# Kernel optimization log

Measured on AMD Instinct MI355X. Metric: run time of the kernel, lower is better.

## Reference

```python
import jax, jax.numpy as jnp
import numpy as np

NEG_SLOPE = 0.1

def _leaky(x):
    return jnp.where(x >= 0, x, NEG_SLOPE * x)

def setup_inputs() -> dict:
    key = jax.random.key(0)
    ks = jax.random.split(key, 16)
    B, N, H, W, C = 4, 128, 32, 32, 64
    inp = {
        "image": jax.random.normal(ks[0], (B, 3, H, W), dtype=jnp.float32),
        "coords": jax.random.uniform(ks[1], (B, N, 2), dtype=jnp.float32),
        "w1": jax.random.normal(ks[2], (C, 7), dtype=jnp.float32) * 0.2,
        "b1": jax.random.normal(ks[3], (C,), dtype=jnp.float32) * 0.05,
        "w2": jax.random.normal(ks[4], (C, C), dtype=jnp.float32) * 0.1,
        "b2": jax.random.normal(ks[5], (C,), dtype=jnp.float32) * 0.05,
        "w3": jax.random.normal(ks[6], (C, C), dtype=jnp.float32) * 0.1,
        "b3": jax.random.normal(ks[7], (C,), dtype=jnp.float32) * 0.05,
        "w4": jax.random.normal(ks[8], (C, C), dtype=jnp.float32) * 0.1,
        "b4": jax.random.normal(ks[9], (C,), dtype=jnp.float32) * 0.05,
        "w5": jax.random.normal(ks[10], (C, C), dtype=jnp.float32) * 0.1,
        "b5": jax.random.normal(ks[11], (C,), dtype=jnp.float32) * 0.05,
        "wl": jax.random.normal(ks[12], (3, C), dtype=jnp.float32) * 0.1,
        "bl": jax.random.normal(ks[13], (3,), dtype=jnp.float32) * 0.05,
    }
    return inp

def reference(image, coords, w1, b1, w2, b2, w3, b3, w4, b4, w5, b5, wl, bl):
    B, C_img, H, W = image.shape
    _, N, D = coords.shape
    # position encoding: channel 0 = row/(H-1), channel 1 = col/(W-1)
    row = (jnp.arange(H, dtype=jnp.float32) / (H - 1))[:, None] * jnp.ones((1, W), jnp.float32)
    col = jnp.ones((H, 1), jnp.float32) * (jnp.arange(W, dtype=jnp.float32) / (W - 1))[None, :]
    pos = jnp.stack([row, col], axis=0)  # [2,H,W]
    # x5: [B,5,H,W] = image ++ pos
    x5 = jnp.concatenate([image, jnp.broadcast_to(pos[None], (B, 2, H, W))], axis=1)
    # First 1x1 conv: split weight into image/pos part (5 ch) and coord part (2 ch);
    # avoids materializing the expanded [B*N,7,H,W] input (same math as conv on concat).
    img_part = jnp.einsum('oc,bchw->bohw', w1[:, :5], x5)          # [B,c,H,W]
    crd_part = jnp.einsum('od,bnd->bno', w1[:, 5:], coords)         # [B,N,c]
    h = _leaky(img_part[:, None] + crd_part[:, :, :, None, None] + b1[None, None, :, None, None])  # [B,N,c,H,W]
    for wi, bi in ((w2, b2), (w3, b3), (w4, b4), (w5, b5)):
        h = _leaky(jnp.einsum('oc,bnchw->bnohw', wi, h) + bi[None, None, :, None, None])
    pooled = jnp.mean(h, axis=(-2, -1))                             # [B,N,c] (AdaptiveAvgPool2d(1,1)+Flatten)
    pred = jax.nn.sigmoid(jnp.einsum('oc,bnc->bno', wl, pooled) + bl)  # [B,N,3]
    return jnp.transpose(pred, (0, 2, 1))                           # [B,3,N]
```

## Files before the change

### kernel.cpp

```cpp
#include <hip/hip_runtime.h>
#include <math.h>


typedef float  f32x4  __attribute__((ext_vector_type(4)));
typedef f32x4  f32x4a __attribute__((may_alias));
typedef __bf16 bf16x4 __attribute__((ext_vector_type(4)));
typedef bf16x4 bf16x4a __attribute__((may_alias));
typedef short  s16x4  __attribute__((ext_vector_type(4)));

static __device__ __forceinline__ f32x4 MFMA16(bf16x4 a, bf16x4 b, f32x4 c) {
    return __builtin_amdgcn_mfma_f32_16x16x16bf16_1k(
        __builtin_bit_cast(s16x4, a), __builtin_bit_cast(s16x4, b), c, 0, 0, 0);
}

static __device__ __forceinline__ bf16x4 cvt4(f32x4 v) {
    bf16x4 r;
    r[0] = (__bf16)v[0]; r[1] = (__bf16)v[1];
    r[2] = (__bf16)v[2]; r[3] = (__bf16)v[3];
    return r;
}

__global__ __launch_bounds__(512, 2) void mlp_mfma_kernel(
    const float* __restrict__ image,
    const float* __restrict__ coords,
    const float* __restrict__ w1, const float* __restrict__ b1,
    const float* __restrict__ w2, const float* __restrict__ b2,
    const float* __restrict__ w3, const float* __restrict__ b3,
    const float* __restrict__ w4, const float* __restrict__ b4,
    const float* __restrict__ w5, const float* __restrict__ b5,
    const float* __restrict__ wl, const float* __restrict__ bl,
    float* __restrict__ out)
{
    __shared__ __align__(16) __bf16 WF[16384];
    __shared__ __align__(16) float  POOL[8][64];
    __shared__ float BL[320];

    const int tid  = threadIdx.x;
    const int wave = tid >> 6;
    const int lane = tid & 63;
    const int c15  = lane & 15;
    const int q    = lane >> 4;
    const int bn   = blockIdx.x;
    const int b    = bn >> 7;

    const float* Ws[4] = {w2, w3, w4, w5};

    {
        const int l  = wave >> 1;
        const int f0 = (wave & 1) * 8;
        const float* Wsrc = Ws[l];
        #pragma unroll
        for (int i = 0; i < 8; ++i) {
            const int f  = f0 + i;
            const int mt = f >> 2, ks = f & 3;
            f32x4 v = *(const f32x4a*)(Wsrc + (mt * 16 + c15) * 64 + ks * 16 + 4 * q);
            *(bf16x4a*)&WF[((l * 16 + f) * 64 + lane) * 4] = cvt4(v);
        }
    }
    if (tid < 64) {
        BL[tid]       = b1[tid];
        BL[64 + tid]  = b2[tid];
        BL[128 + tid] = b3[tid];
        BL[192 + tid] = b4[tid];
        BL[256 + tid] = b5[tid];
    }
    __syncthreads();

    bf16x4 a1[4];
    #pragma unroll
    for (int mt = 0; mt < 4; ++mt)
        #pragma unroll
        for (int j = 0; j < 4; ++j) {
            const int k = 4 * q + j;
            float v = (k < 7) ? w1[(mt * 16 + c15) * 7 + k] : 0.0f;
            a1[mt][j] = (__bf16)v;
        }

    const float cx = coords[2 * bn + 0];
    const float cy = coords[2 * bn + 1];
    const float* img = image + b * 3072;

    const float inv31 = 1.0f / 31.0f;
    const bool  q0  = (q == 0);
    const float g0e = (q == 1) ? (float)c15 * inv31        : 0.0f;
    const float g0o = (q == 1) ? (float)(c15 + 16) * inv31 : 0.0f;
    const float g1  = (q == 1) ? cx : 0.0f;
    const float g2  = (q == 1) ? cy : 0.0f;

    f32x4 pool[4];
    #pragma unroll
    for (int mt = 0; mt < 4; ++mt) pool[mt] = (f32x4){0.f, 0.f, 0.f, 0.f};

    float p0, p1, p2;
    {
        const int hw = wave * 128 + c15;
        p0 = img[hw]; p1 = img[1024 + hw]; p2 = img[2048 + hw];
    }

    #pragma unroll 1
    for (int t = 0; t < 8; ++t) {
        const float rowv = (float)(wave * 4 + (t >> 1)) * inv31;
        const float f0 = q0 ? p0 : ((t & 1) ? g0o : g0e);
        const float f1 = q0 ? p1 : g1;
        const float f2 = q0 ? p2 : g2;
        const float f3 = q0 ? rowv : 0.0f;
        bf16x4 B1;
        B1[0] = (__bf16)f0; B1[1] = (__bf16)f1;
        B1[2] = (__bf16)f2; B1[3] = (__bf16)f3;

        {
            const int tt = (t < 7) ? (t + 1) : 7;
            const int hw = wave * 128 + tt * 16 + c15;
            p0 = img[hw]; p1 = img[1024 + hw]; p2 = img[2048 + hw];
        }

        f32x4 acc[4];
        #pragma unroll
        for (int mt = 0; mt < 4; ++mt)
            acc[mt] = *(const f32x4a*)&BL[mt * 16 + 4 * q];
        #pragma unroll
        for (int mt = 0; mt < 4; ++mt)
            acc[mt] = MFMA16(a1[mt], B1, acc[mt]);

        #pragma unroll
        for (int l = 0; l < 4; ++l) {
            bf16x4 Bf[4];
            #pragma unroll
            for (int mt = 0; mt < 4; ++mt) {
                f32x4 v = acc[mt];
                #pragma unroll
                for (int r = 0; r < 4; ++r) v[r] = fmaxf(v[r], 0.1f * v[r]);
                Bf[mt] = cvt4(v);
            }
            #pragma unroll
            for (int mt = 0; mt < 4; ++mt)
                acc[mt] = *(const f32x4a*)&BL[(l + 1) * 64 + mt * 16 + 4 * q];
            #pragma unroll
            for (int ks = 0; ks < 4; ++ks) {
                bf16x4 af[4];
                #pragma unroll
                for (int mt = 0; mt < 4; ++mt)
                    af[mt] = *(const bf16x4a*)
                        &WF[((l * 16 + mt * 4 + ks) * 64 + lane) * 4];
                #pragma unroll
                for (int mt = 0; mt < 4; ++mt)
                    acc[mt] = MFMA16(af[mt], Bf[ks], acc[mt]);
            }
        }

        #pragma unroll
        for (int mt = 0; mt < 4; ++mt)
            #pragma unroll
            for (int r = 0; r < 4; ++r) {
                const float v = acc[mt][r];
                pool[mt][r] += fmaxf(v, 0.1f * v);
            }
    }

    #pragma unroll
    for (int mt = 0; mt < 4; ++mt)
        #pragma unroll
        for (int r = 0; r < 4; ++r) {
            float v = pool[mt][r];
            v += __shfl_xor(v, 1, 64);
            v += __shfl_xor(v, 2, 64);
            v += __shfl_xor(v, 4, 64);
            v += __shfl_xor(v, 8, 64);
            pool[mt][r] = v;
        }
    if (c15 == 0) {
        #pragma unroll
        for (int mt = 0; mt < 4; ++mt)
            *(f32x4a*)&POOL[wave][mt * 16 + 4 * q] = pool[mt];
    }

    __syncthreads();

    if (tid < 64) {
        const int c = tid;
        float s = 0.0f;
        #pragma unroll
        for (int w = 0; w < 8; ++w) s += POOL[w][c];
        const float p = s * (1.0f / 1024.0f);
        float s0 = wl[c] * p;
        float s1 = wl[64 + c] * p;
        float s2 = wl[128 + c] * p;
        #pragma unroll
        for (int off = 32; off > 0; off >>= 1) {
            s0 += __shfl_down(s0, off, 64);
            s1 += __shfl_down(s1, off, 64);
            s2 += __shfl_down(s2, off, 64);
        }
        if (c == 0) {
            const int n = bn & 127;
            out[(b * 3 + 0) * 128 + n] = 1.0f / (1.0f + expf(-(bl[0] + s0)));
            out[(b * 3 + 1) * 128 + n] = 1.0f / (1.0f + expf(-(bl[1] + s1)));
            out[(b * 3 + 2) * 128 + n] = 1.0f / (1.0f + expf(-(bl[2] + s2)));
        }
    }
}

extern "C" void kernel_launch(void* const* d_in, const int* in_sizes, int n_in,
                              void* d_out, int out_size, void* d_ws, size_t ws_size,
                              hipStream_t stream) {
    const float* image  = (const float*)d_in[0];
    const float* coords = (const float*)d_in[1];
    const float* w1 = (const float*)d_in[2];
    const float* b1 = (const float*)d_in[3];
    const float* w2 = (const float*)d_in[4];
    const float* b2 = (const float*)d_in[5];
    const float* w3 = (const float*)d_in[6];
    const float* b3 = (const float*)d_in[7];
    const float* w4 = (const float*)d_in[8];
    const float* b4 = (const float*)d_in[9];
    const float* w5 = (const float*)d_in[10];
    const float* b5 = (const float*)d_in[11];
    const float* wl = (const float*)d_in[12];
    const float* bl = (const float*)d_in[13];
    float* out = (float*)d_out;

    mlp_mfma_kernel<<<dim3(512), dim3(512), 0, stream>>>(
        image, coords, w1, b1, w2, b2, w3, b3, w4, b4, w5, b5, wl, bl, out);
}
```

Measured before the change: 134.2 us.

## Halve block size and process two pixel tiles per wave to reuse weight fragments

```diff
diff --git a/kernel.cpp b/kernel.cpp
--- a/kernel.cpp
+++ b/kernel.cpp
@@ -20,7 +20,7 @@
     return r;
 }
 
-__global__ __launch_bounds__(512, 2) void mlp_mfma_kernel(
+__global__ __launch_bounds__(256, 2) void mlp_mfma_kernel(
     const float* __restrict__ image,
     const float* __restrict__ coords,
     const float* __restrict__ w1, const float* __restrict__ b1,
@@ -32,7 +32,7 @@
     float* __restrict__ out)
 {
     __shared__ __align__(16) __bf16 WF[16384];
-    __shared__ __align__(16) float  POOL[8][64];
+    __shared__ __align__(16) float  POOL[4][64];
     __shared__ float BL[320];
 
     const int tid  = threadIdx.x;
@@ -46,15 +46,12 @@
     const float* Ws[4] = {w2, w3, w4, w5};
 
     {
-        const int l  = wave >> 1;
-        const int f0 = (wave & 1) * 8;
-        const float* Wsrc = Ws[l];
-        #pragma unroll
-        for (int i = 0; i < 8; ++i) {
-            const int f  = f0 + i;
+        const float* Wsrc = Ws[wave];
+        #pragma unroll
+        for (int f = 0; f < 16; ++f) {
             const int mt = f >> 2, ks = f & 3;
             f32x4 v = *(const f32x4a*)(Wsrc + (mt * 16 + c15) * 64 + ks * 16 + 4 * q);
-            *(bf16x4a*)&WF[((l * 16 + f) * 64 + lane) * 4] = cvt4(v);
+            *(bf16x4a*)&WF[((wave * 16 + f) * 64 + lane) * 4] = cvt4(v);
         }
     }
     if (tid < 64) {
@@ -81,60 +78,72 @@
     const float* img = image + b * 3072;
 
     const float inv31 = 1.0f / 31.0f;
-    const bool  q0  = (q == 0);
-    const float g0e = (q == 1) ? (float)c15 * inv31        : 0.0f;
-    const float g0o = (q == 1) ? (float)(c15 + 16) * inv31 : 0.0f;
-    const float g1  = (q == 1) ? cx : 0.0f;
-    const float g2  = (q == 1) ? cy : 0.0f;
+    const bool  q0 = (q == 0);
+    const float colf0 = (q == 1) ? (float)c15 * inv31        : 0.0f;
+    const float colf1 = (q == 1) ? (float)(c15 + 16) * inv31 : 0.0f;
+    const float g1 = (q == 1) ? cx : 0.0f;
+    const float g2 = (q == 1) ? cy : 0.0f;
 
     f32x4 pool[4];
     #pragma unroll
     for (int mt = 0; mt < 4; ++mt) pool[mt] = (f32x4){0.f, 0.f, 0.f, 0.f};
 
-    float p0, p1, p2;
-    {
-        const int hw = wave * 128 + c15;
-        p0 = img[hw]; p1 = img[1024 + hw]; p2 = img[2048 + hw];
+    float pc[2][3];
+    #pragma unroll
+    for (int ntl = 0; ntl < 2; ++ntl) {
+        const int hw = wave * 256 + ntl * 16 + c15;
+        pc[ntl][0] = img[hw]; pc[ntl][1] = img[1024 + hw]; pc[ntl][2] = img[2048 + hw];
     }
 
     #pragma unroll 1
     for (int t = 0; t < 8; ++t) {
-        const float rowv = (float)(wave * 4 + (t >> 1)) * inv31;
-        const float f0 = q0 ? p0 : ((t & 1) ? g0o : g0e);
-        const float f1 = q0 ? p1 : g1;
-        const float f2 = q0 ? p2 : g2;
-        const float f3 = q0 ? rowv : 0.0f;
-        bf16x4 B1;
-        B1[0] = (__bf16)f0; B1[1] = (__bf16)f1;
-        B1[2] = (__bf16)f2; B1[3] = (__bf16)f3;
-
+        const float rowv = q0 ? (float)(wave * 8 + t) * inv31 : 0.0f;
+        bf16x4 B1[2];
+        #pragma unroll
+        for (int ntl = 0; ntl < 2; ++ntl) {
+            B1[ntl][0] = (__bf16)(q0 ? pc[ntl][0] : (ntl ? colf1 : colf0));
+            B1[ntl][1] = (__bf16)(q0 ? pc[ntl][1] : g1);
+            B1[ntl][2] = (__bf16)(q0 ? pc[ntl][2] : g2);
+            B1[ntl][3] = (__bf16)rowv;
+        }
+
+        if (t < 7) {
+            #pragma unroll
+            for (int ntl = 0; ntl < 2; ++ntl) {
+                const int hw = wave * 256 + (t + 1) * 32 + ntl * 16 + c15;
+                pc[ntl][0] = img[hw]; pc[ntl][1] = img[1024 + hw]; pc[ntl][2] = img[2048 + hw];
+            }
+        }
+
+        f32x4 acc[2][4];
         {
-            const int tt = (t < 7) ? (t + 1) : 7;
-            const int hw = wave * 128 + tt * 16 + c15;
-            p0 = img[hw]; p1 = img[1024 + hw]; p2 = img[2048 + hw];
-        }
-
-        f32x4 acc[4];
-        #pragma unroll
-        for (int mt = 0; mt < 4; ++mt)
-            acc[mt] = *(const f32x4a*)&BL[mt * 16 + 4 * q];
-        #pragma unroll
-        for (int mt = 0; mt < 4; ++mt)
-            acc[mt] = MFMA16(a1[mt], B1, acc[mt]);
+            f32x4 bv[4];
+            #pragma unroll
+            for (int mt = 0; mt < 4; ++mt)
+                bv[mt] = *(const f32x4a*)&BL[mt * 16 + 4 * q];
+            #pragma unroll
+            for (int mt = 0; mt < 4; ++mt) {
+                acc[0][mt] = MFMA16(a1[mt], B1[0], bv[mt]);
+                acc[1][mt] = MFMA16(a1[mt], B1[1], bv[mt]);
+            }
+        }
 
         #pragma unroll
         for (int l = 0; l < 4; ++l) {
-            bf16x4 Bf[4];
-            #pragma unroll
-            for (int mt = 0; mt < 4; ++mt) {
-                f32x4 v = acc[mt];
-                #pragma unroll
-                for (int r = 0; r < 4; ++r) v[r] = fmaxf(v[r], 0.1f * v[r]);
-                Bf[mt] = cvt4(v);
-            }
+            bf16x4 Bf[2][4];
+            #pragma unroll
+            for (int ntl = 0; ntl < 2; ++ntl)
+                #pragma unroll
+                for (int mt = 0; mt < 4; ++mt) {
+                    f32x4 v = acc[ntl][mt];
+                    #pragma unroll
+                    for (int r = 0; r < 4; ++r) v[r] = fmaxf(v[r], 0.1f * v[r]);
+                    Bf[ntl][mt] = cvt4(v);
+                }
+            f32x4 bv[4];
             #pragma unroll
             for (int mt = 0; mt < 4; ++mt)
-                acc[mt] = *(const f32x4a*)&BL[(l + 1) * 64 + mt * 16 + 4 * q];
+                bv[mt] = *(const f32x4a*)&BL[(l + 1) * 64 + mt * 16 + 4 * q];
             #pragma unroll
             for (int ks = 0; ks < 4; ++ks) {
                 bf16x4 af[4];
@@ -143,18 +152,24 @@
                     af[mt] = *(const bf16x4a*)
                         &WF[((l * 16 + mt * 4 + ks) * 64 + lane) * 4];
                 #pragma unroll
-                for (int mt = 0; mt < 4; ++mt)
-                    acc[mt] = MFMA16(af[mt], Bf[ks], acc[mt]);
+                for (int mt = 0; mt < 4; ++mt) {
+                    acc[0][mt] = MFMA16(af[mt], Bf[0][ks],
+                                        (ks == 0) ? bv[mt] : acc[0][mt]);
+                    acc[1][mt] = MFMA16(af[mt], Bf[1][ks],
+                                        (ks == 0) ? bv[mt] : acc[1][mt]);
+                }
             }
         }
 
         #pragma unroll
-        for (int mt = 0; mt < 4; ++mt)
-            #pragma unroll
-            for (int r = 0; r < 4; ++r) {
-                const float v = acc[mt][r];
-                pool[mt][r] += fmaxf(v, 0.1f * v);
-            }
+        for (int ntl = 0; ntl < 2; ++ntl)
+            #pragma unroll
+            for (int mt = 0; mt < 4; ++mt)
+                #pragma unroll
+                for (int r = 0; r < 4; ++r) {
+                    const float v = acc[ntl][mt][r];
+                    pool[mt][r] += fmaxf(v, 0.1f * v);
+                }
     }
 
     #pragma unroll
@@ -180,7 +195,7 @@
         const int c = tid;
         float s = 0.0f;
         #pragma unroll
-        for (int w = 0; w < 8; ++w) s += POOL[w][c];
+        for (int w = 0; w < 4; ++w) s += POOL[w][c];
         const float p = s * (1.0f / 1024.0f);
         float s0 = wl[c] * p;
         float s1 = wl[64 + c] * p;
@@ -219,6 +234,6 @@
     const float* bl = (const float*)d_in[13];
     float* out = (float*)d_out;
 
-    mlp_mfma_kernel<<<dim3(512), dim3(512), 0, stream>>>(
+    mlp_mfma_kernel<<<dim3(512), dim3(256), 0, stream>>>(
         image, coords, w1, b1, w2, b2, w3, b3, w4, b4, w5, b5, wl, bl, out);
 }
```

New measurement: 134.2 us. Within noise of the previous version (-0.0%).
